# Optimization experiments

Measured on AMD Instinct MI355X. Metric: run time of the kernel, lower is better.

## Reference

```python
import jax, jax.numpy as jnp
import numpy as np

EPS = 1e-5


def _edge_conv(x, W, gamma, beta, k):
    """x: (B,N,C); W: (O,2C). Returns (B,N,O)."""
    xx = jnp.sum(x * x, axis=2, keepdims=True)                 # (B,N,1)
    inner = jnp.einsum('bnc,bmc->bnm', x, x)                   # (B,N,N)
    dist = xx + jnp.swapaxes(xx, 1, 2) - 2.0 * inner           # squared dists
    idx = jax.lax.top_k(-dist, k)[1]                           # (B,N,k) smallest dists
    nbr = jax.vmap(lambda xb, ib: xb[ib])(x, idx)              # (B,N,k,C) gather
    xi = jnp.broadcast_to(x[:, :, None, :], nbr.shape)
    edge = jnp.concatenate([nbr - xi, xi], axis=-1)            # (B,N,k,2C)
    out = jnp.einsum('bnkc,oc->bnko', edge, W)                 # 1x1 conv (per-edge linear)
    mean = jnp.mean(out, axis=(0, 1, 2))                       # BatchNorm2d (training stats)
    var = jnp.var(out, axis=(0, 1, 2))
    out = (out - mean) / jnp.sqrt(var + EPS) * gamma + beta
    return jnp.max(jax.nn.relu(out), axis=2)                   # max over k -> (B,N,O)


def _layernorm(x, g, b):
    mu = jnp.mean(x, axis=-1, keepdims=True)
    v = jnp.var(x, axis=-1, keepdims=True)
    return (x - mu) / jnp.sqrt(v + EPS) * g + b


def setup_inputs() -> dict:
    key = jax.random.key(0)
    ks = jax.random.split(key, 12)
    B, N = 8, 2048
    C1, C2, C3, C4 = 64, 64, 128, 256
    feat = C1 + C2 + C3 + C4              # 512
    fc_in = 2 * feat                      # max+avg -> 1024
    H, L = 512, 256

    def w(k_, shape):
        fan_in = shape[-1]
        return jax.random.normal(k_, shape, dtype=jnp.float32) * (1.0 / np.sqrt(fan_in))

    return {
        'points': jax.random.normal(ks[0], (B, N, 3), dtype=jnp.float32),
        'W1': w(ks[1], (C1, 6)),  'g1': jnp.ones(C1), 'b1': jnp.zeros(C1),
        'W2': w(ks[2], (C2, 2 * C1)), 'g2': jnp.ones(C2), 'b2': jnp.zeros(C2),
        'W3': w(ks[3], (C3, 2 * C2)), 'g3': jnp.ones(C3), 'b3': jnp.zeros(C3),
        'W4': w(ks[4], (C4, 2 * C3)), 'g4': jnp.ones(C4), 'b4': jnp.zeros(C4),
        'fc1_w': w(ks[5], (H, fc_in)), 'fc1_b': jnp.zeros(H),
        'ln1_g': jnp.ones(H), 'ln1_b': jnp.zeros(H),
        'fc2_w': w(ks[6], (L, H)), 'fc2_b': jnp.zeros(L),
        'ln2_g': jnp.ones(L), 'ln2_b': jnp.zeros(L),
        'k': 20,
    }


def reference(points, W1, g1, b1, W2, g2, b2, W3, g3, b3, W4, g4, b4,
              fc1_w, fc1_b, ln1_g, ln1_b, fc2_w, fc2_b, ln2_g, ln2_b, k):
    x1 = _edge_conv(points, W1, g1, b1, k)   # (B,N,64)
    x2 = _edge_conv(x1, W2, g2, b2, k)       # (B,N,64)
    x3 = _edge_conv(x2, W3, g3, b3, k)       # (B,N,128)
    x4 = _edge_conv(x3, W4, g4, b4, k)       # (B,N,256)
    feat = jnp.concatenate([x1, x2, x3, x4], axis=-1)          # (B,N,512)
    g = jnp.concatenate([jnp.max(feat, axis=1), jnp.mean(feat, axis=1)], axis=-1)  # (B,1024)
    h = g @ fc1_w.T + fc1_b
    h = jax.nn.relu(_layernorm(h, ln1_g, ln1_b))
    z = h @ fc2_w.T + fc2_b
    return _layernorm(z, ln2_g, ln2_b)       # (B,256)
```

## Files before the change

### kernel.cpp

```cpp
#include <hip/hip_runtime.h>
#include <cstdint>
#include <cstddef>

static constexpr int Bb = 8;
static constexpr int Nn = 2048;
static constexpr int Kn = 20;
static constexpr float EPSV = 1e-5f;


struct TransJobs {
    const float* in[6];
    float* out[6];
    int R[6];
    int Cc[6];
};

__global__ void transpose_all_kernel(TransJobs tj) {
    int m = blockIdx.y;
    int i = blockIdx.x * 256 + threadIdx.x;
    int total = tj.R[m] * tj.Cc[m];
    if (i < total) {
        int r = i / tj.Cc[m], c = i % tj.Cc[m];
        tj.out[m][(size_t)c * tj.R[m] + r] = tj.in[m][i];
    }
}

using half8 = __attribute__((ext_vector_type(8))) _Float16;
using f32x16 = __attribute__((ext_vector_type(16))) float;


template<int C, int O>
__global__ void prep_kernel(const float* __restrict__ x, const float* __restrict__ wt,
                            float* __restrict__ z1, float* __restrict__ z2,
                            float* __restrict__ xx, float4* __restrict__ xp,
                            float* __restrict__ zp) {
    const int blk = blockIdx.x;
    const int tid = threadIdx.x;
    if (blk >= 1088) {
        zp[(blk - 1088) * 256 + tid] = 0.f;
        return;
    }
    if (blk >= 1024) {
        int i = (blk - 1024) * 256 + tid;
        const float* xr = x + (size_t)i * C;
        float s = 0.f;
        for (int c = 0; c < C; ++c) { float v = xr[c]; s += v * v; }
        xx[i] = s;
        if (C == 3) xp[i] = make_float4(xr[0], xr[1], xr[2], s);
        return;
    }
    constexpr int TP = 16;
    constexpr int G = 256 / O;
    constexpr int PP = TP / G;
    const int p0 = blk * TP;
    const int oo = tid % O;
    const int g = tid / O;
    __shared__ float xs[TP][(C < 4) ? 4 : C];
    for (int e = tid; e < TP * C; e += 256) {
        int p = e / C, c = e % C;
        xs[p][c] = x[(size_t)(p0 + p) * C + c];
    }
    __syncthreads();
    float a1[PP], a2[PP];
#pragma unroll
    for (int p = 0; p < PP; ++p) { a1[p] = 0.f; a2[p] = 0.f; }
    for (int c = 0; c < C; ++c) {
        float w1 = wt[(size_t)c * O + oo];
        float w2 = wt[(size_t)(C + c) * O + oo];
#pragma unroll
        for (int p = 0; p < PP; ++p) {
            float xv = xs[g * PP + p][c];
            a1[p] = fmaf(xv, w1, a1[p]);
            a2[p] = fmaf(xv, w2, a2[p]);
        }
    }
#pragma unroll
    for (int p = 0; p < PP; ++p) {
        size_t row = (size_t)(p0 + g * PP + p) * O + oo;
        z1[row] = a1[p];
        z2[row] = a2[p];
    }
}


template<int C>
__global__ void slim2_prep_kernel(const float* __restrict__ x,
                                  float* __restrict__ xx, float* __restrict__ zp) {
    const int blk = blockIdx.x;
    const int tid = threadIdx.x;
    if (blk < 64) {
        int i = blk * 256 + tid;
        const float* xr = x + (size_t)i * C;
        float s = 0.f;
        for (int c = 0; c < C; ++c) { float v = xr[c]; s += v * v; }
        xx[i] = s;
        return;
    }
    zp[(blk - 64) * 256 + tid] = 0.f;
}


template<int C, int O>
__global__ __launch_bounds__(256, 2)
void zmfma_kernel(const float* __restrict__ x, const float* __restrict__ w,
                  float* __restrict__ z1, float* __restrict__ z2) {
    static_assert(C % 32 == 0 && (2 * O) % 128 == 0 && O >= 64, "tiling");
    constexpr int CT = 32;
    const int i0 = blockIdx.x * 128;
    const int j0 = blockIdx.y * 128;
    const int tid = threadIdx.x;
    const int lane = tid & 63;
    const int wv = tid >> 6;
    const int wr = wv >> 1, wc = wv & 1;

    __shared__ __align__(16) unsigned char smem[32768];
    _Float16* const AH = (_Float16*)smem;
    _Float16* const AL = AH + 4096;
    _Float16* const BH = AH + 8192;
    _Float16* const BL = AH + 12288;

    int sga[4];
    const float* sgs[4];
#pragma unroll
    for (int q = 0; q < 4; ++q) {
        int g = tid + 256 * q;
        int pnt = (g >> 2) & 127;
        int cb8 = g & 3;
        sga[q] = cb8 * 128 + (pnt & ~7) + ((pnt + 2 * cb8) & 7);
        if (q < 2) {
            sgs[q] = x + (size_t)(i0 + pnt) * C + cb8 * 8;
        } else {
            int gcol = j0 + pnt;
            int s = (gcol >= O) ? 1 : 0;
            int o = gcol - s * O;
            sgs[q] = w + (size_t)o * (2 * C) + s * C + cb8 * 8;
        }
    }

    int fa[2][2], fb[2][2];
#pragma unroll
    for (int ks = 0; ks < 2; ++ks)
#pragma unroll
        for (int mi = 0; mi < 2; ++mi) {
            int t8 = ks * 2 + (lane >> 5);
            int pa = wr * 64 + mi * 32 + (lane & 31);
            int pb = wc * 64 + mi * 32 + (lane & 31);
            fa[ks][mi] = t8 * 128 + (pa & ~7) + ((pa + 2 * t8) & 7);
            fb[ks][mi] = t8 * 128 + (pb & ~7) + ((pb + 2 * t8) & 7);
        }

    f32x16 ahh[2][2] = {};
    f32x16 axx[2][2] = {};

    for (int c0 = 0; c0 < C; c0 += CT) {
#pragma unroll
        for (int q = 0; q < 4; ++q) {
            const float4 f0 = *(const float4*)(sgs[q] + c0);
            const float4 f1 = *(const float4*)(sgs[q] + c0 + 4);
            float v[8] = {f0.x, f0.y, f0.z, f0.w, f1.x, f1.y, f1.z, f1.w};
            half8 hv, lv;
#pragma unroll
            for (int e = 0; e < 8; ++e) {
                _Float16 h = (_Float16)v[e];
                hv[e] = h;
                lv[e] = (_Float16)((v[e] - (float)h) * 4096.f);
            }
            _Float16* dh = (q < 2) ? AH : BH;
            _Float16* dl = (q < 2) ? AL : BL;
            *(half8*)(dh + sga[q] * 8) = hv;
            *(half8*)(dl + sga[q] * 8) = lv;
        }
        __syncthreads();
#pragma unroll
        for (int ks = 0; ks < 2; ++ks) {
            half8 ah[2], al[2], bh[2], bl[2];
#pragma unroll
            for (int mi = 0; mi < 2; ++mi) {
                ah[mi] = *(const half8*)(AH + fa[ks][mi] * 8);
                al[mi] = *(const half8*)(AL + fa[ks][mi] * 8);
                bh[mi] = *(const half8*)(BH + fb[ks][mi] * 8);
                bl[mi] = *(const half8*)(BL + fb[ks][mi] * 8);
            }
#pragma unroll
            for (int mi = 0; mi < 2; ++mi)
#pragma unroll
                for (int ni = 0; ni < 2; ++ni) {
                    ahh[mi][ni] = __builtin_amdgcn_mfma_f32_32x32x16_f16(ah[mi], bh[ni], ahh[mi][ni], 0, 0, 0);
                    axx[mi][ni] = __builtin_amdgcn_mfma_f32_32x32x16_f16(ah[mi], bl[ni], axx[mi][ni], 0, 0, 0);
                    axx[mi][ni] = __builtin_amdgcn_mfma_f32_32x32x16_f16(al[mi], bh[ni], axx[mi][ni], 0, 0, 0);
                }
        }
        __syncthreads();
    }

#pragma unroll
    for (int mi = 0; mi < 2; ++mi)
#pragma unroll
        for (int ni = 0; ni < 2; ++ni) {
            const int cb = wc * 64 + ni * 32;
            const int s = ((j0 + cb) >= O) ? 1 : 0;
            float* outp = s ? z2 : z1;
            const int o = j0 + cb - s * O + (lane & 31);
#pragma unroll
            for (int r = 0; r < 16; ++r) {
                int row = i0 + wr * 64 + mi * 32 + (r & 3) + 8 * (r >> 2) + 4 * (lane >> 5);
                outp[(size_t)row * O + o] = fmaf(axx[mi][ni][r], 2.44140625e-4f, ahh[mi][ni][r]);
            }
        }
}


template<int C>
__global__ __launch_bounds__(256, 2)
void gram_dist_kernel(const float* __restrict__ x, const float* __restrict__ xx,
                      float* __restrict__ dist, int b0, size_t dstride) {
    static_assert(C % 32 == 0, "CT=32 tiling");
    constexpr int CT = 32;
    const int b = b0 + blockIdx.z;
    int p = blockIdx.x, rblk = 0;
    while (p >= 16 - rblk) { p -= 16 - rblk; ++rblk; }
    const int cblk = rblk + p;
    const int i0 = rblk * 128, j0 = cblk * 128;
    const int tid = threadIdx.x;
    const int lane = tid & 63;
    const int wv = tid >> 6;
    const int wr = wv >> 1, wc = wv & 1;

    __shared__ __align__(16) unsigned char smem[67584];
    _Float16* const AH = (_Float16*)smem;
    _Float16* const AL = AH + 4096;
    _Float16* const BH = AH + 8192;
    _Float16* const BL = AH + 12288;
    float (*T2)[132] = (float (*)[132])smem;

    const float* xb = x + (size_t)b * Nn * C;
    int sga[4];
    const float* sgs[4];
#pragma unroll
    for (int q = 0; q < 4; ++q) {
        int g = tid + 256 * q;
        int pnt = (g >> 2) & 127;
        int cb8 = g & 3;
        sga[q] = cb8 * 128 + (pnt & ~7) + ((pnt + 2 * cb8) & 7);
        sgs[q] = xb + (size_t)(((q < 2) ? i0 : j0) + pnt) * C + cb8 * 8;
    }

    int fa[2][2], fb[2][2];
#pragma unroll
    for (int ks = 0; ks < 2; ++ks)
#pragma unroll
        for (int mi = 0; mi < 2; ++mi) {
            int t8 = ks * 2 + (lane >> 5);
            int pa = wr * 64 + mi * 32 + (lane & 31);
            int pb = wc * 64 + mi * 32 + (lane & 31);
            fa[ks][mi] = t8 * 128 + (pa & ~7) + ((pa + 2 * t8) & 7);
            fb[ks][mi] = t8 * 128 + (pb & ~7) + ((pb + 2 * t8) & 7);
        }

    f32x16 ahh[2][2] = {};
    f32x16 axx[2][2] = {};

    for (int c0 = 0; c0 < C; c0 += CT) {
#pragma unroll
        for (int q = 0; q < 4; ++q) {
            const float4 f0 = *(const float4*)(sgs[q] + c0);
            const float4 f1 = *(const float4*)(sgs[q] + c0 + 4);
            float v[8] = {f0.x, f0.y, f0.z, f0.w, f1.x, f1.y, f1.z, f1.w};
            half8 hv, lv;
#pragma unroll
            for (int e = 0; e < 8; ++e) {
                _Float16 h = (_Float16)v[e];
                hv[e] = h;
                lv[e] = (_Float16)((v[e] - (float)h) * 4096.f);
            }
            _Float16* dh = (q < 2) ? AH : BH;
            _Float16* dl = (q < 2) ? AL : BL;
            *(half8*)(dh + sga[q] * 8) = hv;
            *(half8*)(dl + sga[q] * 8) = lv;
        }
        __syncthreads();
#pragma unroll
        for (int ks = 0; ks < 2; ++ks) {
            half8 ah[2], al[2], bh[2], bl[2];
#pragma unroll
            for (int mi = 0; mi < 2; ++mi) {
                ah[mi] = *(const half8*)(AH + fa[ks][mi] * 8);
                al[mi] = *(const half8*)(AL + fa[ks][mi] * 8);
                bh[mi] = *(const half8*)(BH + fb[ks][mi] * 8);
                bl[mi] = *(const half8*)(BL + fb[ks][mi] * 8);
            }
#pragma unroll
            for (int mi = 0; mi < 2; ++mi)
#pragma unroll
                for (int ni = 0; ni < 2; ++ni) {
                    ahh[mi][ni] = __builtin_amdgcn_mfma_f32_32x32x16_f16(ah[mi], bh[ni], ahh[mi][ni], 0, 0, 0);
                    axx[mi][ni] = __builtin_amdgcn_mfma_f32_32x32x16_f16(ah[mi], bl[ni], axx[mi][ni], 0, 0, 0);
                    axx[mi][ni] = __builtin_amdgcn_mfma_f32_32x32x16_f16(al[mi], bh[ni], axx[mi][ni], 0, 0, 0);
                }
        }
        __syncthreads();
    }

    const float* xxb = xx + (size_t)b * Nn;
    float xi[2][16];
#pragma unroll
    for (int mi = 0; mi < 2; ++mi)
#pragma unroll
        for (int g = 0; g < 4; ++g) {
            float4 t4 = *(const float4*)(xxb + i0 + wr * 64 + mi * 32 + 4 * (lane >> 5) + 8 * g);
            xi[mi][g * 4 + 0] = t4.x; xi[mi][g * 4 + 1] = t4.y;
            xi[mi][g * 4 + 2] = t4.z; xi[mi][g * 4 + 3] = t4.w;
        }
    float xj[2];
#pragma unroll
    for (int ni = 0; ni < 2; ++ni) xj[ni] = xxb[j0 + wc * 64 + ni * 32 + (lane & 31)];

    float* db = dist + (size_t)blockIdx.z * dstride;

    if (cblk == rblk) {
#pragma unroll
        for (int mi = 0; mi < 2; ++mi)
#pragma unroll
            for (int ni = 0; ni < 2; ++ni) {
                const int col = j0 + wc * 64 + ni * 32 + (lane & 31);
#pragma unroll
                for (int r = 0; r < 16; ++r) {
                    int row = i0 + wr * 64 + mi * 32 + (r & 3) + 8 * (r >> 2) + 4 * (lane >> 5);
                    float inner = fmaf(axx[mi][ni][r], 2.44140625e-4f, ahh[mi][ni][r]);
                    db[(size_t)row * Nn + col] = xi[mi][r] + xj[ni] - 2.f * inner;
                }
            }
    } else {
#pragma unroll
        for (int mi = 0; mi < 2; ++mi)
#pragma unroll
            for (int ni = 0; ni < 2; ++ni) {
                const int mrow = wc * 64 + ni * 32 + (lane & 31);
#pragma unroll
                for (int r = 0; r < 16; ++r) {
                    int mcol = wr * 64 + mi * 32 + (r & 3) + 8 * (r >> 2) + 4 * (lane >> 5);
                    float inner = fmaf(axx[mi][ni][r], 2.44140625e-4f, ahh[mi][ni][r]);
                    T2[mrow][mcol] = xi[mi][r] + xj[ni] - 2.f * inner;
                }
            }
        __syncthreads();
#pragma unroll
        for (int mi = 0; mi < 2; ++mi)
#pragma unroll
            for (int ni = 0; ni < 2; ++ni) {
                const int col = j0 + wc * 64 + ni * 32 + (lane & 31);
#pragma unroll
                for (int r = 0; r < 16; ++r) {
                    int row = i0 + wr * 64 + mi * 32 + (r & 3) + 8 * (r >> 2) + 4 * (lane >> 5);
                    float inner = fmaf(axx[mi][ni][r], 2.44140625e-4f, ahh[mi][ni][r]);
                    db[(size_t)row * Nn + col] = xi[mi][r] + xj[ni] - 2.f * inner;
                }
            }
        const int rr = tid >> 3;
        const int c4 = (tid & 7) * 4;
#pragma unroll
        for (int m = 0; m < 4; ++m) {
            const int row = m * 32 + rr;
            float* orow = db + (size_t)(j0 + row) * Nn + i0;
#pragma unroll
            for (int s = 0; s < 4; ++s)
                *(float4*)(orow + c4 + s * 32) = *(const float4*)&T2[row][c4 + s * 32];
        }
    }
}


template<int CTRL>
__device__ __forceinline__ float dpp_min_step(float v) {
    int x = __float_as_int(v);
    int y = __builtin_amdgcn_update_dpp(x, x, CTRL, 0xf, 0xf, false);
    return fminf(v, __int_as_float(y));
}

__device__ __forceinline__ float wave_min64(float v) {
    v = dpp_min_step<0x111>(v);
    v = dpp_min_step<0x112>(v);
    v = dpp_min_step<0x114>(v);
    v = dpp_min_step<0x118>(v);
    v = dpp_min_step<0x142>(v);
    v = dpp_min_step<0x143>(v);
    return __int_as_float(__builtin_amdgcn_readlane(__float_as_int(v), 63));
}

__device__ __forceinline__ float pack_key(float v, int m) {
    return __int_as_float((__float_as_int(v) & ~31) | m);
}

#define TOP4_INS(v)                                                               \
    {                                                                             \
        bool l3 = (v) < tv3;                                                      \
        if (l3) {                                                                 \
            bool l2 = (v) < tv2;                                                  \
            bool l1 = (v) < tv1;                                                  \
            bool l0 = (v) < tv0;                                                  \
            tv3 = l2 ? tv2 : (v);                                                 \
            tv2 = l2 ? (l1 ? tv1 : (v)) : tv2;                                    \
            tv1 = l1 ? (l0 ? tv0 : (v)) : tv1;                                    \
            tv0 = l0 ? (v) : tv0;                                                 \
        }                                                                         \
    }

__device__ __forceinline__ void top4_build(const float4* __restrict__ dr4, int lane,
                                           float lvk,
                                           float& tv0, float& tv1, float& tv2, float& tv3) {
    tv0 = tv1 = tv2 = tv3 = 3e38f;
#pragma unroll
    for (int q = 0; q < 8; ++q) {
        float4 f = dr4[q * 64 + lane];
        float vv[4] = {f.x, f.y, f.z, f.w};
#pragma unroll
        for (int c = 0; c < 4; ++c) {
            float vk = pack_key(vv[c], q * 4 + c);
            if (vk > lvk) TOP4_INS(vk)
        }
    }
}

#define TOPK_ROUNDS(REBUILD, DECODE)                                              \
    int myj = 0;                                                                  \
    for (int t = 0; t < Kn; ++t) {                                                \
        float bv = wave_min64(tv0);                                               \
        unsigned long long tied = __ballot(tv0 == bv);                            \
        int wl = (int)(__ffsll((long long)tied) - 1);                             \
        int bm = __float_as_int(bv) & 31;                                         \
        int bj = (DECODE);                                                        \
        if (lane == t) myj = bj;                                                  \
        if (tv0 == bv && lane == wl) {                                            \
            tv0 = tv1; tv1 = tv2; tv2 = tv3; tv3 = 3e38f;                         \
            if (tv0 == 3e38f) { REBUILD; }                                        \
        }                                                                         \
    }                                                                             \
    if (lane < Kn) orow[lane] = myj;

__global__ void topk_kernel(const float* __restrict__ dist, int* __restrict__ idxo,
                            int b0, size_t dstride, int rows_per_batch_only) {
    const int w = threadIdx.x >> 6;
    const int lane = threadIdx.x & 63;
    const int lin = blockIdx.x * 4 + w;
    int bz, i;
    if (rows_per_batch_only) { bz = 0; i = lin; }
    else { bz = lin >> 11; i = lin & (Nn - 1); }
    const int b = b0 + bz;
    const float4* dr4 = (const float4*)(dist + (size_t)bz * dstride + (size_t)i * Nn);

    float tv0, tv1, tv2, tv3;
    top4_build(dr4, lane, -3e38f, tv0, tv1, tv2, tv3);

    int* orow = idxo + ((size_t)b * Nn + i) * Kn;
    TOPK_ROUNDS(top4_build(dr4, lane, bv, tv0, tv1, tv2, tv3),
                (bm >> 2) * 256 + wl * 4 + (bm & 3))
}


__device__ __forceinline__ void top4_build_c3(const float4* __restrict__ xpb,
                                              float xi0, float xi1, float xi2, float xxi,
                                              int lane, float lvk,
                                              float& tv0, float& tv1, float& tv2, float& tv3) {
    tv0 = tv1 = tv2 = tv3 = 3e38f;
#pragma unroll
    for (int m = 0; m < 32; ++m) {
        float4 f = xpb[m * 64 + lane];
        float acc = 0.f;
        acc = fmaf(xi0, f.x, acc);
        acc = fmaf(xi1, f.y, acc);
        acc = fmaf(xi2, f.z, acc);
        float v = xxi + f.w - 2.f * acc;
        float vk = pack_key(v, m);
        if (vk > lvk) TOP4_INS(vk)
    }
}

__global__ void topk_c3_kernel(const float4* __restrict__ xp, int* __restrict__ idxo,
                               int b0, int rows_per_batch_only) {
    const int w = threadIdx.x >> 6;
    const int lane = threadIdx.x & 63;
    const int lin = blockIdx.x * 4 + w;
    int bz, i;
    if (rows_per_batch_only) { bz = 0; i = lin; }
    else { bz = lin >> 11; i = lin & (Nn - 1); }
    const int b = b0 + bz;
    const float4* xpb = xp + (size_t)b * Nn;
    const float4 fi = xpb[i];
    const float xi0 = fi.x, xi1 = fi.y, xi2 = fi.z, xxi = fi.w;

    float tv0, tv1, tv2, tv3;
    top4_build_c3(xpb, xi0, xi1, xi2, xxi, lane, -3e38f, tv0, tv1, tv2, tv3);

    int* orow = idxo + ((size_t)b * Nn + i) * Kn;
    TOPK_ROUNDS(top4_build_c3(xpb, xi0, xi1, xi2, xxi, lane, bv, tv0, tv1, tv2, tv3),
                bm * 64 + wl)
}


template<int O>
__global__ void edge_stats_kernel(const float* __restrict__ z1, const float* __restrict__ z2,
                                  const int* __restrict__ idx,
                                  float* __restrict__ vmax, float* __restrict__ vmin,
                                  float* __restrict__ ssum, float* __restrict__ ssq) {
    constexpr int TPP = O / 4;
    constexpr int PPB = 256 / TPP;
    const int p0 = blockIdx.x * PPB;
    const int tid = threadIdx.x;
    const int q = tid % TPP;
    const int p = tid / TPP;
    const int oo = q * 4;
    __shared__ int jl[PPB][Kn];
    for (int e = tid; e < PPB * Kn; e += 256)
        jl[e / Kn][e % Kn] = idx[(size_t)(p0 + e / Kn) * Kn + (e % Kn)];
    __syncthreads();
    const int bi = p0 + p;
    const int b = bi >> 11;
    const float4 zi1 = *(const float4*)(z1 + (size_t)bi * O + oo);
    const float4 zi2 = *(const float4*)(z2 + (size_t)bi * O + oo);
    float ax = zi2.x - zi1.x, ay = zi2.y - zi1.y, az = zi2.z - zi1.z, aw = zi2.w - zi1.w;
    float mxx = -3e38f, mxy = -3e38f, mxz = -3e38f, mxw = -3e38f;
    float mnx = 3e38f, mny = 3e38f, mnz = 3e38f, mnw = 3e38f;
    float sx = 0.f, sy = 0.f, sz = 0.f, sw = 0.f;
    float qx = 0.f, qy = 0.f, qz = 0.f, qw = 0.f;
    const float* zbase = z1 + ((size_t)b * Nn) * O + oo;
#pragma unroll
    for (int kk = 0; kk < Kn; ++kk) {
        int j = jl[p][kk];
        float4 v = *(const float4*)(zbase + (size_t)j * O);
        v.x += ax; v.y += ay; v.z += az; v.w += aw;
        mxx = fmaxf(mxx, v.x); mxy = fmaxf(mxy, v.y); mxz = fmaxf(mxz, v.z); mxw = fmaxf(mxw, v.w);
        mnx = fminf(mnx, v.x); mny = fminf(mny, v.y); mnz = fminf(mnz, v.z); mnw = fminf(mnw, v.w);
        sx += v.x; sy += v.y; sz += v.z; sw += v.w;
        qx = fmaf(v.x, v.x, qx); qy = fmaf(v.y, v.y, qy);
        qz = fmaf(v.z, v.z, qz); qw = fmaf(v.w, v.w, qw);
    }
    float4 mx4 = make_float4(mxx, mxy, mxz, mxw);
    float4 mn4 = make_float4(mnx, mny, mnz, mnw);
    *(float4*)(vmax + (size_t)bi * O + oo) = mx4;
    *(float4*)(vmin + (size_t)bi * O + oo) = mn4;
    __shared__ float4 ssm[256], sqq[256];
    ssm[tid] = make_float4(sx, sy, sz, sw);
    sqq[tid] = make_float4(qx, qy, qz, qw);
    __syncthreads();
    if (p == 0) {
#pragma unroll 4
        for (int pp = 1; pp < PPB; ++pp) {
            float4 s4 = ssm[pp * TPP + q];
            float4 q4 = sqq[pp * TPP + q];
            sx += s4.x; sy += s4.y; sz += s4.z; sw += s4.w;
            qx += q4.x; qy += q4.y; qz += q4.z; qw += q4.w;
        }
        int slot = blockIdx.x & 63;
        atomicAdd(&ssum[slot * O + oo + 0], sx);
        atomicAdd(&ssum[slot * O + oo + 1], sy);
        atomicAdd(&ssum[slot * O + oo + 2], sz);
        atomicAdd(&ssum[slot * O + oo + 3], sw);
        atomicAdd(&ssq[slot * O + oo + 0], qx);
        atomicAdd(&ssq[slot * O + oo + 1], qy);
        atomicAdd(&ssq[slot * O + oo + 2], qz);
        atomicAdd(&ssq[slot * O + oo + 3], qw);
    }
}


template<int O>
__global__ void apply_pool_kernel(const float* __restrict__ vmax, const float* __restrict__ vmin,
                                  const float* __restrict__ ssum, const float* __restrict__ ssq,
                                  const float* __restrict__ gamma, const float* __restrict__ beta,
                                  float* __restrict__ xout,
                                  float* __restrict__ pmax, float* __restrict__ psum, int obase) {
    constexpr int TPP = O / 4;
    constexpr int PP2 = 256 / TPP;
    constexpr int S = 128 / PP2;
    const int chunk = blockIdx.x;
    const int b = blockIdx.y;
    const int tid = threadIdx.x;
    const int q = tid % TPP;
    const int g = tid / TPP;
    const int oo = q * 4;
    __shared__ __align__(16) float lsc[O], lsh[O];
    for (int o = tid; o < O; o += 256) {
        float s = 0.f, qq = 0.f;
        for (int sl = 0; sl < 64; ++sl) { s += ssum[sl * O + o]; qq += ssq[sl * O + o]; }
        const float cnt = (float)Bb * (float)Nn * (float)Kn;
        float mu = s / cnt;
        float var = qq / cnt - mu * mu;
        float sc_ = gamma[o] / sqrtf(var + EPSV);
        lsc[o] = sc_;
        lsh[o] = beta[o] - mu * sc_;
    }
    __syncthreads();
    const float4 sc = *(const float4*)(lsc + oo);
    const float4 sh = *(const float4*)(lsh + oo);
    float pmx = -3e38f, pmy = -3e38f, pmz = -3e38f, pmw = -3e38f;
    float psx = 0.f, psy = 0.f, psz = 0.f, psw = 0.f;
    const int n0 = chunk * 128;
    for (int s = 0; s < S; ++s) {
        int n = n0 + g + s * PP2;
        size_t ix = ((size_t)b * Nn + n) * O + oo;
        float4 vx = *(const float4*)(vmax + ix);
        float4 vn = *(const float4*)(vmin + ix);
        float4 r;
        r.x = fmaxf(fmaf(sc.x >= 0.f ? vx.x : vn.x, sc.x, sh.x), 0.f);
        r.y = fmaxf(fmaf(sc.y >= 0.f ? vx.y : vn.y, sc.y, sh.y), 0.f);
        r.z = fmaxf(fmaf(sc.z >= 0.f ? vx.z : vn.z, sc.z, sh.z), 0.f);
        r.w = fmaxf(fmaf(sc.w >= 0.f ? vx.w : vn.w, sc.w, sh.w), 0.f);
        *(float4*)(xout + ix) = r;
        pmx = fmaxf(pmx, r.x); pmy = fmaxf(pmy, r.y);
        pmz = fmaxf(pmz, r.z); pmw = fmaxf(pmw, r.w);
        psx += r.x; psy += r.y; psz += r.z; psw += r.w;
    }
    __shared__ float4 sm[256], ss2[256];
    sm[tid] = make_float4(pmx, pmy, pmz, pmw);
    ss2[tid] = make_float4(psx, psy, psz, psw);
    __syncthreads();
    if (g == 0) {
#pragma unroll 4
        for (int gg = 1; gg < PP2; ++gg) {
            float4 m4 = sm[gg * TPP + q];
            float4 s4 = ss2[gg * TPP + q];
            pmx = fmaxf(pmx, m4.x); pmy = fmaxf(pmy, m4.y);
            pmz = fmaxf(pmz, m4.z); pmw = fmaxf(pmw, m4.w);
            psx += s4.x; psy += s4.y; psz += s4.z; psw += s4.w;
        }
        size_t pb = ((size_t)b * 16 + chunk) * 512 + obase + oo;
        *(float4*)(pmax + pb) = make_float4(pmx, pmy, pmz, pmw);
        *(float4*)(psum + pb) = make_float4(psx, psy, psz, psw);
    }
}


__global__ void head1_kernel(const float* __restrict__ pmax, const float* __restrict__ psum,
                             const float* __restrict__ fct1, float* __restrict__ hp1) {
    const int ks = blockIdx.x;
    const int b = blockIdx.y;
    const int tid = threadIdx.x;
    __shared__ float gxs[64];
    if (tid < 64) {
        int c = ks * 64 + tid;
        if (c < 512) {
            float mx = -3e38f;
            for (int ch = 0; ch < 16; ++ch)
                mx = fmaxf(mx, pmax[((size_t)b * 16 + ch) * 512 + c]);
            gxs[tid] = mx;
        } else {
            int e = c - 512;
            float s = 0.f;
            for (int ch = 0; ch < 16; ++ch)
                s += psum[((size_t)b * 16 + ch) * 512 + e];
            gxs[tid] = s * (1.f / (float)Nn);
        }
    }
    __syncthreads();
    float h0 = 0.f, h1 = 0.f;
    const float* w = fct1 + (size_t)(ks * 64) * 512;
    for (int c = 0; c < 64; ++c) {
        float gc = gxs[c];
        h0 = fmaf(gc, w[(size_t)c * 512 + tid], h0);
        h1 = fmaf(gc, w[(size_t)c * 512 + tid + 256], h1);
    }
    hp1[((size_t)b * 16 + ks) * 512 + tid] = h0;
    hp1[((size_t)b * 16 + ks) * 512 + tid + 256] = h1;
}

__global__ void head2_kernel(const float* __restrict__ hp1, const float* __restrict__ fc1b,
                             const float* __restrict__ ln1g, const float* __restrict__ ln1b,
                             float* __restrict__ hh) {
    const int b = blockIdx.x;
    const int tid = threadIdx.x;
    __shared__ float red[256];
    float h0 = fc1b[tid], h1 = fc1b[tid + 256];
    for (int ks = 0; ks < 16; ++ks) {
        h0 += hp1[((size_t)b * 16 + ks) * 512 + tid];
        h1 += hp1[((size_t)b * 16 + ks) * 512 + tid + 256];
    }
    red[tid] = h0 + h1;
    __syncthreads();
    for (int st = 128; st > 0; st >>= 1) { if (tid < st) red[tid] += red[tid + st]; __syncthreads(); }
    float mu = red[0] * (1.f / 512.f);
    __syncthreads();
    float d0 = h0 - mu, d1 = h1 - mu;
    red[tid] = d0 * d0 + d1 * d1;
    __syncthreads();
    for (int st = 128; st > 0; st >>= 1) { if (tid < st) red[tid] += red[tid + st]; __syncthreads(); }
    float rs = 1.f / sqrtf(red[0] * (1.f / 512.f) + EPSV);
    hh[(size_t)b * 512 + tid]       = fmaxf(d0 * rs * ln1g[tid] + ln1b[tid], 0.f);
    hh[(size_t)b * 512 + tid + 256] = fmaxf(d1 * rs * ln1g[tid + 256] + ln1b[tid + 256], 0.f);
}

__global__ void head3_kernel(const float* __restrict__ hh, const float* __restrict__ fct2,
                             float* __restrict__ hp2) {
    const int ks = blockIdx.x;
    const int b = blockIdx.y;
    const int tid = threadIdx.x;
    __shared__ float hs[128];
    if (tid < 128) hs[tid] = hh[(size_t)b * 512 + ks * 128 + tid];
    __syncthreads();
    float z = 0.f;
    const float* w = fct2 + (size_t)(ks * 128) * 256;
    for (int c = 0; c < 128; ++c)
        z = fmaf(hs[c], w[(size_t)c * 256 + tid], z);
    hp2[((size_t)b * 4 + ks) * 256 + tid] = z;
}

__global__ void head4_kernel(const float* __restrict__ hp2, const float* __restrict__ fc2b,
                             const float* __restrict__ ln2g, const float* __restrict__ ln2b,
                             float* __restrict__ out) {
    const int b = blockIdx.x;
    const int tid = threadIdx.x;
    __shared__ float red[256];
    float z = fc2b[tid];
    for (int ks = 0; ks < 4; ++ks) z += hp2[((size_t)b * 4 + ks) * 256 + tid];
    red[tid] = z;
    __syncthreads();
    for (int st = 128; st > 0; st >>= 1) { if (tid < st) red[tid] += red[tid + st]; __syncthreads(); }
    float mu2 = red[0] * (1.f / 256.f);
    __syncthreads();
    float dz = z - mu2;
    red[tid] = dz * dz;
    __syncthreads();
    for (int st = 128; st > 0; st >>= 1) { if (tid < st) red[tid] += red[tid + st]; __syncthreads(); }
    float rs2 = 1.f / sqrtf(red[0] * (1.f / 256.f) + EPSV);
    out[b * 256 + tid] = dz * rs2 * ln2g[tid] + ln2b[tid];
}


template<int C, int O>
static void run_layer(const float* x, const float* W, const float* gamma, const float* beta,
                      float* xout, float* DIST, float* XX, float4* XP, int* IDX,
                      float* Z1, float* Z2,
                      float* VMX, float* VMN, float* SSUM, float* SSQ,
                      const float* WT, float* PMAX, float* PSUM, int obase, bool big,
                      hipStream_t stream) {
    if constexpr (C == 3) {
        prep_kernel<C, O><<<1216, 256, 0, stream>>>(x, WT, Z1, Z2, XX, XP, SSUM);
        if (big) {
            topk_c3_kernel<<<Bb * Nn / 4, 256, 0, stream>>>(XP, IDX, 0, 0);
        } else {
            for (int b = 0; b < Bb; ++b)
                topk_c3_kernel<<<Nn / 4, 256, 0, stream>>>(XP, IDX, b, 1);
        }
    } else {
        slim2_prep_kernel<C><<<192, 256, 0, stream>>>(x, XX, SSUM);
        zmfma_kernel<C, O><<<dim3(Bb * Nn / 128, 2 * O / 128), 256, 0, stream>>>(x, W, Z1, Z2);
        if (big) {
            gram_dist_kernel<C><<<dim3(136, 1, Bb), 256, 0, stream>>>(x, XX, DIST, 0, (size_t)Nn * Nn);
            topk_kernel<<<Bb * Nn / 4, 256, 0, stream>>>(DIST, IDX, 0, (size_t)Nn * Nn, 0);
        } else {
            for (int b = 0; b < Bb; ++b) {
                gram_dist_kernel<C><<<dim3(136, 1, 1), 256, 0, stream>>>(x, XX, DIST, b, 0);
                topk_kernel<<<Nn / 4, 256, 0, stream>>>(DIST, IDX, b, 0, 1);
            }
        }
    }
    edge_stats_kernel<O><<<Bb * Nn / (1024 / O), 256, 0, stream>>>(Z1, Z2, IDX, VMX, VMN, SSUM, SSQ);
    apply_pool_kernel<O><<<dim3(16, 8), 256, 0, stream>>>(VMX, VMN, SSUM, SSQ, gamma, beta,
                                                          xout, PMAX, PSUM, obase);
}

extern "C" void kernel_launch(void* const* d_in, const int* in_sizes, int n_in,
                              void* d_out, int out_size, void* d_ws, size_t ws_size,
                              hipStream_t stream) {
    const float* points = (const float*)d_in[0];
    const float* W1 = (const float*)d_in[1];
    const float* g1 = (const float*)d_in[2];
    const float* b1 = (const float*)d_in[3];
    const float* W2 = (const float*)d_in[4];
    const float* g2 = (const float*)d_in[5];
    const float* b2 = (const float*)d_in[6];
    const float* W3 = (const float*)d_in[7];
    const float* g3 = (const float*)d_in[8];
    const float* b3 = (const float*)d_in[9];
    const float* W4 = (const float*)d_in[10];
    const float* g4 = (const float*)d_in[11];
    const float* b4 = (const float*)d_in[12];
    const float* fc1_w = (const float*)d_in[13];
    const float* fc1_b = (const float*)d_in[14];
    const float* ln1g = (const float*)d_in[15];
    const float* ln1b = (const float*)d_in[16];
    const float* fc2_w = (const float*)d_in[17];
    const float* fc2_b = (const float*)d_in[18];
    const float* ln2g = (const float*)d_in[19];
    const float* ln2b = (const float*)d_in[20];

    float* ws = (float*)d_ws;
    const size_t BN = (size_t)Bb * Nn;
    const bool big = ws_size >= (size_t)59826688 * 4;

    size_t off = 0;
    auto take = [&](size_t n) { size_t o = off; off += n; return o; };
    float* DIST = ws + take(big ? (size_t)Bb * Nn * Nn : (size_t)Nn * Nn);
    float* XX   = ws + take(BN);
    float4* XP  = (float4*)(ws + take(BN * 4));
    int*   IDX  = (int*)(ws + take(BN * Kn));
    float* Z1   = ws + take(BN * 256);
    float* Z2   = ws + take(BN * 256);
    float* VMX  = ws + take(BN * 256);
    float* VMN  = ws + take(BN * 256);
    float* SSUM = ws + take(64 * 256);
    float* SSQ  = ws + take(64 * 256);
    float* WT1  = ws + take(384);
    float* WT2  = ws + take(8192);
    float* WT3  = ws + take(16384);
    float* WT4  = ws + take(65536);
    float* FCT1 = ws + take(524288);
    float* FCT2 = ws + take(131072);
    float* X1   = ws + take(BN * 64);
    float* X2   = ws + take(BN * 64);
    float* X3   = ws + take(BN * 128);
    float* X4   = ws + take(BN * 256);
    float* PMAX = ws + take((size_t)Bb * 16 * 512);
    float* PSUM = ws + take((size_t)Bb * 16 * 512);
    (void)WT2; (void)WT3; (void)WT4;

    float* HP1 = DIST;
    float* HH  = DIST + 65536;
    float* HP2 = DIST + 65536 + 4096;

    TransJobs tj;
    tj.in[0] = W1;    tj.out[0] = WT1;  tj.R[0] = 64;  tj.Cc[0] = 6;
    tj.in[1] = fc1_w; tj.out[1] = FCT1; tj.R[1] = 512; tj.Cc[1] = 1024;
    tj.in[2] = fc2_w; tj.out[2] = FCT2; tj.R[2] = 256; tj.Cc[2] = 512;
    transpose_all_kernel<<<dim3(2048, 3), 256, 0, stream>>>(tj);

    run_layer<3, 64>(points, W1, g1, b1, X1, DIST, XX, XP, IDX, Z1, Z2, VMX, VMN, SSUM, SSQ, WT1, PMAX, PSUM, 0, big, stream);
    run_layer<64, 64>(X1, W2, g2, b2, X2, DIST, XX, XP, IDX, Z1, Z2, VMX, VMN, SSUM, SSQ, WT1, PMAX, PSUM, 64, big, stream);
    run_layer<64, 128>(X2, W3, g3, b3, X3, DIST, XX, XP, IDX, Z1, Z2, VMX, VMN, SSUM, SSQ, WT1, PMAX, PSUM, 128, big, stream);
    run_layer<128, 256>(X3, W4, g4, b4, X4, DIST, XX, XP, IDX, Z1, Z2, VMX, VMN, SSUM, SSQ, WT1, PMAX, PSUM, 256, big, stream);

    head1_kernel<<<dim3(16, 8), 256, 0, stream>>>(PMAX, PSUM, FCT1, HP1);
    head2_kernel<<<Bb, 256, 0, stream>>>(HP1, fc1_b, ln1g, ln1b, HH);
    head3_kernel<<<dim3(4, 8), 256, 0, stream>>>(HH, FCT2, HP2);
    head4_kernel<<<Bb, 256, 0, stream>>>(HP2, fc2_b, ln2g, ln2b, (float*)d_out);
}
```

Baseline: 519.4 us.

## Fuse gram-distance, edge matmul and stats zeroing into one launch per layer

Merges the squared-norm prep, zero-init, z-projection MFMA kernel and the pairwise distance kernel into a single heterogeneous launch that dispatches on block index. Norms are now computed per tile inside the gram kernel into shared memory instead of a separate pass. The aim is to remove launch gaps and let the independent z-matmul and gram work fill the GPU concurrently. In exchange, norms are recomputed redundantly per tile, and the fused kernel's shared-memory size is set by the larger gram tile, which may lower occupancy for the zmfma blocks.

Result: slower. 561.5 us (+8.1%).

```diff
diff --git a/kernel.cpp b/kernel.cpp
--- a/kernel.cpp
+++ b/kernel.cpp
@@ -82,38 +82,25 @@
     }
 }
 
-
-template<int C>
-__global__ void slim2_prep_kernel(const float* __restrict__ x,
-                                  float* __restrict__ xx, float* __restrict__ zp) {
-    const int blk = blockIdx.x;
-    const int tid = threadIdx.x;
-    if (blk < 64) {
-        int i = blk * 256 + tid;
-        const float* xr = x + (size_t)i * C;
-        float s = 0.f;
-        for (int c = 0; c < C; ++c) { float v = xr[c]; s += v * v; }
-        xx[i] = s;
-        return;
-    }
-    zp[(blk - 64) * 256 + tid] = 0.f;
+__global__ void zero_stats_kernel(float* __restrict__ zp) {
+    zp[blockIdx.x * 256 + threadIdx.x] = 0.f;
 }
 
 
 template<int C, int O>
-__global__ __launch_bounds__(256, 2)
-void zmfma_kernel(const float* __restrict__ x, const float* __restrict__ w,
-                  float* __restrict__ z1, float* __restrict__ z2) {
-    static_assert(C % 32 == 0 && (2 * O) % 128 == 0 && O >= 64, "tiling");
+__device__ __forceinline__ void zmfma_body(unsigned char* smem,
+                                           const float* __restrict__ x,
+                                           const float* __restrict__ w,
+                                           float* __restrict__ z1, float* __restrict__ z2,
+                                           int bx, int by) {
     constexpr int CT = 32;
-    const int i0 = blockIdx.x * 128;
-    const int j0 = blockIdx.y * 128;
+    const int i0 = bx * 128;
+    const int j0 = by * 128;
     const int tid = threadIdx.x;
     const int lane = tid & 63;
     const int wv = tid >> 6;
     const int wr = wv >> 1, wc = wv & 1;
 
-    __shared__ __align__(16) unsigned char smem[32768];
     _Float16* const AH = (_Float16*)smem;
     _Float16* const AL = AH + 4096;
     _Float16* const BH = AH + 8192;
@@ -209,15 +196,23 @@
         }
 }
 
+template<int C, int O>
+__global__ __launch_bounds__(256, 2)
+void zmfma_kernel(const float* __restrict__ x, const float* __restrict__ w,
+                  float* __restrict__ z1, float* __restrict__ z2) {
+    __shared__ __align__(16) unsigned char smem[32768];
+    zmfma_body<C, O>(smem, x, w, z1, z2, blockIdx.x, blockIdx.y);
+}
+
+
+static constexpr int GRAM_SMEM = 68608;
 
 template<int C>
-__global__ __launch_bounds__(256, 2)
-void gram_dist_kernel(const float* __restrict__ x, const float* __restrict__ xx,
-                      float* __restrict__ dist, int b0, size_t dstride) {
-    static_assert(C % 32 == 0, "CT=32 tiling");
+__device__ __forceinline__ void gram_body(unsigned char* smem,
+                                          const float* __restrict__ xb,
+                                          float* __restrict__ db, int p) {
     constexpr int CT = 32;
-    const int b = b0 + blockIdx.z;
-    int p = blockIdx.x, rblk = 0;
+    int rblk = 0;
     while (p >= 16 - rblk) { p -= 16 - rblk; ++rblk; }
     const int cblk = rblk + p;
     const int i0 = rblk * 128, j0 = cblk * 128;
@@ -226,14 +221,21 @@
     const int wv = tid >> 6;
     const int wr = wv >> 1, wc = wv & 1;
 
-    __shared__ __align__(16) unsigned char smem[67584];
     _Float16* const AH = (_Float16*)smem;
     _Float16* const AL = AH + 4096;
     _Float16* const BH = AH + 8192;
     _Float16* const BL = AH + 12288;
     float (*T2)[132] = (float (*)[132])smem;
-
-    const float* xb = x + (size_t)b * Nn * C;
+    float* const NRM = (float*)(smem + 67584);
+
+    {
+        int row = (tid < 128) ? (i0 + tid) : (j0 + (tid - 128));
+        const float* xr = xb + (size_t)row * C;
+        float s = 0.f;
+        for (int c = 0; c < C; ++c) { float v = xr[c]; s += v * v; }
+        NRM[tid] = s;
+    }
+
     int sga[4];
     const float* sgs[4];
 #pragma unroll
@@ -301,21 +303,18 @@
         __syncthreads();
     }
 
-    const float* xxb = xx + (size_t)b * Nn;
     float xi[2][16];
 #pragma unroll
     for (int mi = 0; mi < 2; ++mi)
 #pragma unroll
         for (int g = 0; g < 4; ++g) {
-            float4 t4 = *(const float4*)(xxb + i0 + wr * 64 + mi * 32 + 4 * (lane >> 5) + 8 * g);
+            float4 t4 = *(const float4*)&NRM[wr * 64 + mi * 32 + 4 * (lane >> 5) + 8 * g];
             xi[mi][g * 4 + 0] = t4.x; xi[mi][g * 4 + 1] = t4.y;
             xi[mi][g * 4 + 2] = t4.z; xi[mi][g * 4 + 3] = t4.w;
         }
     float xj[2];
 #pragma unroll
-    for (int ni = 0; ni < 2; ++ni) xj[ni] = xxb[j0 + wc * 64 + ni * 32 + (lane & 31)];
-
-    float* db = dist + (size_t)blockIdx.z * dstride;
+    for (int ni = 0; ni < 2; ++ni) xj[ni] = NRM[128 + wc * 64 + ni * 32 + (lane & 31)];
 
     if (cblk == rblk) {
 #pragma unroll
@@ -366,6 +365,36 @@
             for (int s = 0; s < 4; ++s)
                 *(float4*)(orow + c4 + s * 32) = *(const float4*)&T2[row][c4 + s * 32];
         }
+    }
+}
+
+template<int C>
+__global__ __launch_bounds__(256, 2)
+void gram_dist_kernel(const float* __restrict__ x, float* __restrict__ dist, int b) {
+    __shared__ __align__(16) unsigned char smem[GRAM_SMEM];
+    gram_body<C>(smem, x + (size_t)b * Nn * C, dist, blockIdx.x);
+}
+
+
+template<int C, int O>
+__global__ __launch_bounds__(256, 2)
+void layer_fused_kernel(const float* __restrict__ x, const float* __restrict__ w,
+                        float* __restrict__ z1, float* __restrict__ z2,
+                        float* __restrict__ dist, float* __restrict__ zp) {
+    __shared__ __align__(16) unsigned char smem[GRAM_SMEM];
+    constexpr int NG = 136 * Bb;
+    constexpr int GX = Bb * Nn / 128;
+    constexpr int NZ = GX * (2 * O / 128);
+    const int blk = blockIdx.x;
+    if (blk < NG) {
+        const int b = blk / 136;
+        const int p = blk - b * 136;
+        gram_body<C>(smem, x + (size_t)b * Nn * C, dist + (size_t)b * Nn * Nn, p);
+    } else if (blk < NG + NZ) {
+        const int t = blk - NG;
+        zmfma_body<C, O>(smem, x, w, z1, z2, t % GX, t / GX);
+    } else {
+        zp[(blk - NG - NZ) * 256 + threadIdx.x] = 0.f;
     }
 }
 
@@ -741,14 +770,15 @@
                 topk_c3_kernel<<<Nn / 4, 256, 0, stream>>>(XP, IDX, b, 1);
         }
     } else {
-        slim2_prep_kernel<C><<<192, 256, 0, stream>>>(x, XX, SSUM);
-        zmfma_kernel<C, O><<<dim3(Bb * Nn / 128, 2 * O / 128), 256, 0, stream>>>(x, W, Z1, Z2);
         if (big) {
-            gram_dist_kernel<C><<<dim3(136, 1, Bb), 256, 0, stream>>>(x, XX, DIST, 0, (size_t)Nn * Nn);
+            constexpr int NB = 136 * Bb + (Bb * Nn / 128) * (2 * O / 128) + 128;
+            layer_fused_kernel<C, O><<<NB, 256, 0, stream>>>(x, W, Z1, Z2, DIST, SSUM);
             topk_kernel<<<Bb * Nn / 4, 256, 0, stream>>>(DIST, IDX, 0, (size_t)Nn * Nn, 0);
         } else {
+            zero_stats_kernel<<<128, 256, 0, stream>>>(SSUM);
+            zmfma_kernel<C, O><<<dim3(Bb * Nn / 128, 2 * O / 128), 256, 0, stream>>>(x, W, Z1, Z2);
             for (int b = 0; b < Bb; ++b) {
-                gram_dist_kernel<C><<<dim3(136, 1, 1), 256, 0, stream>>>(x, XX, DIST, b, 0);
+                gram_dist_kernel<C><<<136, 256, 0, stream>>>(x, DIST, b);
                 topk_kernel<<<Nn / 4, 256, 0, stream>>>(DIST, IDX, b, 0, 1);
             }
         }
```
